# Kernel tuning notes

Hardware: AMD Instinct MI355X
Metric: run time of the kernel (lower is better)

## Reference

```python
import jax, jax.numpy as jnp
import numpy as np

EPS = 1e-6
CONV_P = 3.0
GM_P = 2.0
NUM_NODES = 50000
NUM_EDGES = 600000
NUM_GRAPHS = 512
IN_DIM = 128
HID = 128
OUT_DIM = 64


def _scatter_mean(vals, index, num_segments):
    # scatter_mean with empty segments -> 0 (count clamped to 1)
    s = jax.ops.segment_sum(vals, index, num_segments=num_segments)
    cnt = jax.ops.segment_sum(jnp.ones((vals.shape[0],), vals.dtype), index,
                              num_segments=num_segments)
    return s / jnp.maximum(cnt, 1.0)[:, None]


def _signed_pow(v, p):
    return jnp.sign(v) * (jnp.abs(v) + EPS) ** p


def _spm_conv(x, W, b, src, dst, p):
    h = x @ W.T + b                      # [N, hid] linear
    msg = h[src]                          # gather x_j  [E, hid]
    t = _signed_pow(msg, p)
    pooled = _scatter_mean(t, dst, NUM_NODES)
    return _signed_pow(pooled, 1.0 / p)


def setup_inputs() -> dict:
    key = jax.random.key(0)
    ks = jax.random.split(key, 8)
    x = jax.random.normal(ks[0], (NUM_NODES, IN_DIM), jnp.float32)
    edge_index = jax.random.randint(ks[1], (2, NUM_EDGES), 0, NUM_NODES)
    batch = jnp.sort(jax.random.randint(ks[2], (NUM_NODES,), 0, NUM_GRAPHS))
    s1 = 1.0 / np.sqrt(IN_DIM)
    s2 = 1.0 / np.sqrt(HID)
    W1 = jax.random.uniform(ks[3], (HID, IN_DIM), jnp.float32, -s1, s1)
    b1 = jax.random.uniform(ks[4], (HID,), jnp.float32, -s1, s1)
    W2 = jax.random.uniform(ks[5], (HID, HID), jnp.float32, -s2, s2)
    b2 = jax.random.uniform(ks[6], (HID,), jnp.float32, -s2, s2)
    # final layer: orthogonal-init frozen weight (out_dim=64, hid=128)
    A = jax.random.normal(ks[7], (HID, OUT_DIM), jnp.float32)
    Q, _ = jnp.linalg.qr(A)
    Wout = Q.T                            # [OUT_DIM, HID], orthonormal rows
    bout = jax.random.uniform(jax.random.fold_in(key, 9), (OUT_DIM,),
                              jnp.float32, -s2, s2)
    return {"x": x, "W1": W1, "b1": b1, "W2": W2, "b2": b2,
            "Wout": Wout, "bout": bout, "edge_index": edge_index,
            "batch": batch}


def reference(x, W1, b1, W2, b2, Wout, bout, edge_index, batch):
    src, dst = edge_index[0], edge_index[1]
    h = _spm_conv(x, W1, b1, src, dst, CONV_P)
    h = jax.nn.relu(h)                    # relu between conv layers only
    h = _spm_conv(h, W2, b2, src, dst, CONV_P)
    # global generalized mean pool (signed)
    t = _signed_pow(h, GM_P)
    pooled = _scatter_mean(t, batch, NUM_GRAPHS)
    graph_repr = _signed_pow(pooled, 1.0 / GM_P)   # [G, HID]
    return graph_repr @ Wout.T + bout              # [G, OUT_DIM]
```

## Files before the change

### kernel.cpp

```cpp
#include <hip/hip_runtime.h>
#include <hip/hip_bf16.h>
#include <math.h>

#define N_NODES 50000
#define N_EDGES 600000
#define N_GRAPHS 512
#define DIM 128
#define OUTD 64
#define EPSV 1e-6f
#define BSTRIDE 64

typedef __attribute__((ext_vector_type(8))) short bf16x8;
typedef __attribute__((ext_vector_type(4))) float f32x4;

__device__ __forceinline__ float sgn(float v) {
    return (v > 0.f) ? 1.f : ((v < 0.f) ? -1.f : 0.f);
}

__device__ __forceinline__ float cube_signed(float v) {
    float m = fabsf(v) + EPSV;
    return sgn(v) * m * m * m;
}

__device__ __forceinline__ float cbrt_pos(float m) {
    return exp2f(log2f(m) * (1.0f / 3.0f));
}

__device__ __forceinline__ unsigned short f2bf(float f) {
    unsigned u = __float_as_uint(f);
    unsigned r = (u + 0x7fff + ((u >> 16) & 1)) >> 16;
    return (unsigned short)r;
}

__device__ __forceinline__ float bf2f(unsigned short h) {
    return __uint_as_float(((unsigned)h) << 16);
}


__global__ void prep(const float* __restrict__ W1, const float* __restrict__ W2,
                     unsigned short* __restrict__ W1hi, unsigned short* __restrict__ W1lo,
                     unsigned short* __restrict__ W2hi, unsigned short* __restrict__ W2lo,
                     int* __restrict__ deg,
                     const int* __restrict__ batch, int* __restrict__ gstart) {
    int i = blockIdx.x * blockDim.x + threadIdx.x;
    if (i < N_NODES) deg[i] = 0;
    if (i < DIM * DIM) {
        float w = W1[i];
        unsigned short h = f2bf(w);
        W1hi[i] = h;
        W1lo[i] = f2bf(w - bf2f(h));
        w = W2[i];
        h = f2bf(w);
        W2hi[i] = h;
        W2lo[i] = f2bf(w - bf2f(h));
    }
    if (i <= N_GRAPHS) {
        int lo = 0, hi = N_NODES;
        while (lo < hi) {
            int mid = (lo + hi) >> 1;
            if (batch[mid] < i) lo = mid + 1; else hi = mid;
        }
        gstart[i] = lo;
    }
}


__global__ void bucket_fill(const int* __restrict__ src, const int* __restrict__ dst,
                            int* __restrict__ deg, int* __restrict__ csr, int E) {
    int e = blockIdx.x * blockDim.x + threadIdx.x;
    if (e < E) {
        int d = dst[e];
        int slot = atomicAdd(&deg[d], 1);
        if (slot < BSTRIDE) csr[d * BSTRIDE + slot] = src[e];
    }
}


__global__ __launch_bounds__(256) void linear_cube_mfma(const float* __restrict__ X,
                                                        const unsigned short* __restrict__ Whi,
                                                        const unsigned short* __restrict__ Wlo,
                                                        const float* __restrict__ B,
                                                        unsigned short* __restrict__ T) {
    int wave = threadIdx.x >> 6;
    int lane = threadIdx.x & 63;
    int tile = blockIdx.x * 4 + wave;
    if (tile >= N_NODES / 16) return;
    int n0 = tile * 16;
    int r = lane & 15;
    int g = lane >> 4;

    bf16x8 xh[4], xl[4];
    const float* xrow = X + (size_t)(n0 + r) * DIM + g * 8;
    #pragma unroll
    for (int kb = 0; kb < 4; kb++) {
        float4 a = *(const float4*)(xrow + kb * 32);
        float4 b = *(const float4*)(xrow + kb * 32 + 4);
        float v[8] = {a.x, a.y, a.z, a.w, b.x, b.y, b.z, b.w};
        #pragma unroll
        for (int j = 0; j < 8; j++) {
            unsigned short h = f2bf(v[j]);
            float rem = v[j] - bf2f(h);
            xh[kb][j] = (short)h;
            xl[kb][j] = (short)f2bf(rem);
        }
    }

    #pragma unroll
    for (int ct = 0; ct < 8; ct++) {
        const unsigned short* whbase = Whi + (size_t)(ct * 16 + r) * DIM + g * 8;
        const unsigned short* wlbase = Wlo + (size_t)(ct * 16 + r) * DIM + g * 8;
        f32x4 acc = {0.f, 0.f, 0.f, 0.f};
        #pragma unroll
        for (int kb = 0; kb < 4; kb++) {
            bf16x8 wh = *(const bf16x8*)(whbase + kb * 32);
            bf16x8 wl = *(const bf16x8*)(wlbase + kb * 32);
            acc = __builtin_amdgcn_mfma_f32_16x16x32_bf16(xh[kb], wh, acc, 0, 0, 0);
            acc = __builtin_amdgcn_mfma_f32_16x16x32_bf16(xl[kb], wh, acc, 0, 0, 0);
            acc = __builtin_amdgcn_mfma_f32_16x16x32_bf16(xh[kb], wl, acc, 0, 0, 0);
        }
        float bias = B[ct * 16 + r];
        #pragma unroll
        for (int q = 0; q < 4; q++) {
            int node = g * 4 + q;
            float h = acc[q] + bias;
            T[(size_t)(n0 + node) * DIM + ct * 16 + r] = f2bf(cube_signed(h));
        }
    }
}


__global__ __launch_bounds__(256) void aggregate(const unsigned* __restrict__ T32,
                                                 const int* __restrict__ deg,
                                                 const int* __restrict__ csr,
                                                 float* __restrict__ P, int relu) {
    int nd = blockIdx.x * 4 + (threadIdx.x >> 6);
    if (nd >= N_NODES) return;
    int lane = threadIdx.x & 63;
    int d = deg[nd];
    int cnt = d < BSTRIDE ? d : BSTRIDE;
    const int* bucket = csr + (size_t)nd * BSTRIDE;
    float a0 = 0.f, a1 = 0.f;
    int i = 0;
    for (; i + 4 <= cnt; i += 4) {
        int s0 = bucket[i], s1 = bucket[i + 1], s2 = bucket[i + 2], s3 = bucket[i + 3];
        unsigned u0 = T32[s0 * 64 + lane];
        unsigned u1 = T32[s1 * 64 + lane];
        unsigned u2 = T32[s2 * 64 + lane];
        unsigned u3 = T32[s3 * 64 + lane];
        a0 += __uint_as_float(u0 << 16) + __uint_as_float(u1 << 16)
            + __uint_as_float(u2 << 16) + __uint_as_float(u3 << 16);
        a1 += __uint_as_float(u0 & 0xffff0000u) + __uint_as_float(u1 & 0xffff0000u)
            + __uint_as_float(u2 & 0xffff0000u) + __uint_as_float(u3 & 0xffff0000u);
    }
    for (; i < cnt; i++) {
        unsigned u = T32[bucket[i] * 64 + lane];
        a0 += __uint_as_float(u << 16);
        a1 += __uint_as_float(u & 0xffff0000u);
    }
    float c = (float)(d > 1 ? d : 1);
    float m0 = a0 / c, m1 = a1 / c;
    float r0 = sgn(m0) * cbrt_pos(fabsf(m0) + EPSV);
    float r1 = sgn(m1) * cbrt_pos(fabsf(m1) + EPSV);
    if (relu) { r0 = fmaxf(r0, 0.f); r1 = fmaxf(r1, 0.f); }
    float2* dstp = (float2*)(P + (size_t)nd * DIM + lane * 2);
    *dstp = make_float2(r0, r1);
}


__global__ __launch_bounds__(128) void pool_final(const float* __restrict__ P,
                                                  const int* __restrict__ gstart,
                                                  const float* __restrict__ Wout,
                                                  const float* __restrict__ bout,
                                                  float* __restrict__ out) {
    __shared__ float R[DIM];
    __shared__ float partial[128];
    int g = blockIdx.x, f = threadIdx.x;
    int s = gstart[g], e = gstart[g + 1];
    float acc = 0.f;
    for (int i = s; i < e; i++) {
        float v = P[(size_t)i * DIM + f];
        float m = fabsf(v) + EPSV;
        acc += sgn(v) * m * m;
    }
    int cnt = e - s;
    float c = (float)(cnt > 1 ? cnt : 1);
    float mean = acc / c;
    R[f] = sgn(mean) * sqrtf(fabsf(mean) + EPSV);
    __syncthreads();

    int o = f & 63;
    int half = f >> 6;
    const float4* W4 = (const float4*)Wout + o * 32 + half * 16;
    const float4* R4 = (const float4*)R + half * 16;
    float a = 0.f;
    #pragma unroll
    for (int k = 0; k < 16; k++) {
        float4 w = W4[k];
        float4 r = R4[k];
        a += r.x * w.x + r.y * w.y + r.z * w.z + r.w * w.w;
    }
    partial[f] = a;
    __syncthreads();
    if (f < OUTD) out[(size_t)g * OUTD + f] = bout[f] + partial[f] + partial[f + 64];
}


extern "C" void kernel_launch(void* const* d_in, const int* in_sizes, int n_in,
                              void* d_out, int out_size, void* d_ws, size_t ws_size,
                              hipStream_t stream) {
    const float* x    = (const float*)d_in[0];
    const float* W1   = (const float*)d_in[1];
    const float* b1   = (const float*)d_in[2];
    const float* W2   = (const float*)d_in[3];
    const float* b2   = (const float*)d_in[4];
    const float* Wout = (const float*)d_in[5];
    const float* bout = (const float*)d_in[6];
    const int* edge   = (const int*)d_in[7];
    const int* batch  = (const int*)d_in[8];
    const int* srcp = edge;
    const int* dstp = edge + N_EDGES;
    float* out = (float*)d_out;

    char* ws = (char*)d_ws;
    size_t off = 0;
    auto alloc = [&](size_t bytes) -> char* {
        char* p = ws + off;
        off += (bytes + 255) / 256 * 256;
        return p;
    };
    unsigned short* T = (unsigned short*)alloc((size_t)N_NODES * DIM * 2);
    float* P        = (float*)alloc((size_t)N_NODES * DIM * 4);
    int*   deg      = (int*)alloc((size_t)N_NODES * 4);
    int*   csr      = (int*)alloc((size_t)N_NODES * BSTRIDE * 4);
    int*   gstart   = (int*)alloc((size_t)(N_GRAPHS + 1) * 4);
    unsigned short* W1hi = (unsigned short*)alloc((size_t)DIM * DIM * 2);
    unsigned short* W1lo = (unsigned short*)alloc((size_t)DIM * DIM * 2);
    unsigned short* W2hi = (unsigned short*)alloc((size_t)DIM * DIM * 2);
    unsigned short* W2lo = (unsigned short*)alloc((size_t)DIM * DIM * 2);

    prep<<<(N_NODES + 255) / 256, 256, 0, stream>>>(W1, W2, W1hi, W1lo, W2hi, W2lo,
                                                    deg, batch, gstart);
    bucket_fill<<<(N_EDGES + 255) / 256, 256, 0, stream>>>(srcp, dstp, deg, csr, N_EDGES);

    const int TILES = N_NODES / 16;
    const int LBLK = (TILES + 3) / 4;
    const int ABLK = (N_NODES + 3) / 4;
    linear_cube_mfma<<<LBLK, 256, 0, stream>>>(x, W1hi, W1lo, b1, T);
    aggregate<<<ABLK, 256, 0, stream>>>((const unsigned*)T, deg, csr, P, 1);
    linear_cube_mfma<<<LBLK, 256, 0, stream>>>(P, W2hi, W2lo, b2, T);
    aggregate<<<ABLK, 256, 0, stream>>>((const unsigned*)T, deg, csr, P, 0);
    pool_final<<<N_GRAPHS, 128, 0, stream>>>(P, gstart, Wout, bout, out);
}
```

Before: 219.4 us.

## Fuse first aggregation with second linear layer and merge setup kernels

Adds a kernel that gathers and mean-pools neighbour features for 16 nodes into shared memory, applies cube root and ReLU, then runs the second MFMA linear plus cube on that tile directly. This removes the fp32 round trip of the intermediate P between layers and one launch. Setup is also folded into one build kernel that handles bucket fill and weight splitting in separate block ranges, with deg zeroed by a memset. Each fused block now does both gather and MFMA work, which may change occupancy and latency hiding, and a second T buffer is used so the gather reads and the writes go to different arrays.

```diff
diff --git a/kernel.cpp b/kernel.cpp
--- a/kernel.cpp
+++ b/kernel.cpp
@@ -9,6 +9,8 @@
 #define OUTD 64
 #define EPSV 1e-6f
 #define BSTRIDE 64
+#define EBLK 2344
+#define PREP_BLK 64
 
 typedef __attribute__((ext_vector_type(8))) short bf16x8;
 typedef __attribute__((ext_vector_type(4))) float f32x4;
@@ -37,41 +39,40 @@
 }
 
 
-__global__ void prep(const float* __restrict__ W1, const float* __restrict__ W2,
-                     unsigned short* __restrict__ W1hi, unsigned short* __restrict__ W1lo,
-                     unsigned short* __restrict__ W2hi, unsigned short* __restrict__ W2lo,
-                     int* __restrict__ deg,
-                     const int* __restrict__ batch, int* __restrict__ gstart) {
-    int i = blockIdx.x * blockDim.x + threadIdx.x;
-    if (i < N_NODES) deg[i] = 0;
-    if (i < DIM * DIM) {
-        float w = W1[i];
-        unsigned short h = f2bf(w);
-        W1hi[i] = h;
-        W1lo[i] = f2bf(w - bf2f(h));
-        w = W2[i];
-        h = f2bf(w);
-        W2hi[i] = h;
-        W2lo[i] = f2bf(w - bf2f(h));
-    }
-    if (i <= N_GRAPHS) {
-        int lo = 0, hi = N_NODES;
-        while (lo < hi) {
-            int mid = (lo + hi) >> 1;
-            if (batch[mid] < i) lo = mid + 1; else hi = mid;
-        }
-        gstart[i] = lo;
-    }
-}
-
-
-__global__ void bucket_fill(const int* __restrict__ src, const int* __restrict__ dst,
-                            int* __restrict__ deg, int* __restrict__ csr, int E) {
-    int e = blockIdx.x * blockDim.x + threadIdx.x;
-    if (e < E) {
-        int d = dst[e];
-        int slot = atomicAdd(&deg[d], 1);
-        if (slot < BSTRIDE) csr[d * BSTRIDE + slot] = src[e];
+__global__ void build(const int* __restrict__ src, const int* __restrict__ dst,
+                      int* __restrict__ deg, int* __restrict__ csr,
+                      const float* __restrict__ W1, const float* __restrict__ W2,
+                      unsigned short* __restrict__ W1hi, unsigned short* __restrict__ W1lo,
+                      unsigned short* __restrict__ W2hi, unsigned short* __restrict__ W2lo,
+                      const int* __restrict__ batch, int* __restrict__ gstart) {
+    int b = blockIdx.x;
+    if (b < EBLK) {
+        int e = b * 256 + threadIdx.x;
+        if (e < N_EDGES) {
+            int d = dst[e];
+            int slot = atomicAdd(&deg[d], 1);
+            if (slot < BSTRIDE) csr[d * BSTRIDE + slot] = src[e];
+        }
+    } else {
+        int i = (b - EBLK) * 256 + threadIdx.x;
+        if (i < DIM * DIM) {
+            float w = W1[i];
+            unsigned short h = f2bf(w);
+            W1hi[i] = h;
+            W1lo[i] = f2bf(w - bf2f(h));
+            w = W2[i];
+            h = f2bf(w);
+            W2hi[i] = h;
+            W2lo[i] = f2bf(w - bf2f(h));
+        }
+        if (i <= N_GRAPHS) {
+            int lo = 0, hi = N_NODES;
+            while (lo < hi) {
+                int mid = (lo + hi) >> 1;
+                if (batch[mid] < i) lo = mid + 1; else hi = mid;
+            }
+            gstart[i] = lo;
+        }
     }
 }
 
@@ -129,10 +130,95 @@
 }
 
 
+__global__ __launch_bounds__(256) void agg_linear_cube(const unsigned* __restrict__ T32,
+                                                       const int* __restrict__ deg,
+                                                       const int* __restrict__ csr,
+                                                       const unsigned short* __restrict__ Whi,
+                                                       const unsigned short* __restrict__ Wlo,
+                                                       const float* __restrict__ B,
+                                                       unsigned short* __restrict__ Tout) {
+    __shared__ float Pl[16][132];
+    int wave = threadIdx.x >> 6;
+    int lane = threadIdx.x & 63;
+    int n0 = blockIdx.x * 16;
+
+    #pragma unroll
+    for (int q = 0; q < 4; q++) {
+        int nd = n0 + wave * 4 + q;
+        int d = deg[nd];
+        int cnt = d < BSTRIDE ? d : BSTRIDE;
+        const int* bucket = csr + (size_t)nd * BSTRIDE;
+        float a0 = 0.f, a1 = 0.f;
+        int i = 0;
+        for (; i + 4 <= cnt; i += 4) {
+            int s0 = bucket[i], s1 = bucket[i + 1], s2 = bucket[i + 2], s3 = bucket[i + 3];
+            unsigned u0 = T32[s0 * 64 + lane];
+            unsigned u1 = T32[s1 * 64 + lane];
+            unsigned u2 = T32[s2 * 64 + lane];
+            unsigned u3 = T32[s3 * 64 + lane];
+            a0 += __uint_as_float(u0 << 16) + __uint_as_float(u1 << 16)
+                + __uint_as_float(u2 << 16) + __uint_as_float(u3 << 16);
+            a1 += __uint_as_float(u0 & 0xffff0000u) + __uint_as_float(u1 & 0xffff0000u)
+                + __uint_as_float(u2 & 0xffff0000u) + __uint_as_float(u3 & 0xffff0000u);
+        }
+        for (; i < cnt; i++) {
+            unsigned u = T32[bucket[i] * 64 + lane];
+            a0 += __uint_as_float(u << 16);
+            a1 += __uint_as_float(u & 0xffff0000u);
+        }
+        float c = (float)(d > 1 ? d : 1);
+        float m0 = a0 / c, m1 = a1 / c;
+        float r0 = fmaxf(sgn(m0) * cbrt_pos(fabsf(m0) + EPSV), 0.f);
+        float r1 = fmaxf(sgn(m1) * cbrt_pos(fabsf(m1) + EPSV), 0.f);
+        int row = wave * 4 + q;
+        Pl[row][2 * lane]     = r0;
+        Pl[row][2 * lane + 1] = r1;
+    }
+    __syncthreads();
+
+    int r = lane & 15;
+    int g = lane >> 4;
+    bf16x8 xh[4], xl[4];
+    #pragma unroll
+    for (int kb = 0; kb < 4; kb++) {
+        const float* prow = &Pl[r][kb * 32 + g * 8];
+        #pragma unroll
+        for (int j = 0; j < 8; j++) {
+            float v = prow[j];
+            unsigned short h = f2bf(v);
+            xh[kb][j] = (short)h;
+            xl[kb][j] = (short)f2bf(v - bf2f(h));
+        }
+    }
+    #pragma unroll
+    for (int ctl = 0; ctl < 2; ctl++) {
+        int ct = wave * 2 + ctl;
+        const unsigned short* whbase = Whi + (size_t)(ct * 16 + r) * DIM + g * 8;
+        const unsigned short* wlbase = Wlo + (size_t)(ct * 16 + r) * DIM + g * 8;
+        f32x4 acc = {0.f, 0.f, 0.f, 0.f};
+        #pragma unroll
+        for (int kb = 0; kb < 4; kb++) {
+            bf16x8 wh = *(const bf16x8*)(whbase + kb * 32);
+            bf16x8 wl = *(const bf16x8*)(wlbase + kb * 32);
+            acc = __builtin_amdgcn_mfma_f32_16x16x32_bf16(xh[kb], wh, acc, 0, 0, 0);
+            acc = __builtin_amdgcn_mfma_f32_16x16x32_bf16(xl[kb], wh, acc, 0, 0, 0);
+            acc = __builtin_amdgcn_mfma_f32_16x16x32_bf16(xh[kb], wl, acc, 0, 0, 0);
+        }
+        float bias = B[ct * 16 + r];
+        #pragma unroll
+        for (int q = 0; q < 4; q++) {
+            int node = g * 4 + q;
+            float h = acc[q] + bias;
+            Tout[(size_t)(n0 + node) * DIM + ct * 16 + r] = f2bf(cube_signed(h));
+        }
+    }
+}
+
+
 __global__ __launch_bounds__(256) void aggregate(const unsigned* __restrict__ T32,
                                                  const int* __restrict__ deg,
                                                  const int* __restrict__ csr,
-                                                 float* __restrict__ P, int relu) {
+                                                 float* __restrict__ P) {
     int nd = blockIdx.x * 4 + (threadIdx.x >> 6);
     if (nd >= N_NODES) return;
     int lane = threadIdx.x & 63;
@@ -161,7 +247,6 @@
     float m0 = a0 / c, m1 = a1 / c;
     float r0 = sgn(m0) * cbrt_pos(fabsf(m0) + EPSV);
     float r1 = sgn(m1) * cbrt_pos(fabsf(m1) + EPSV);
-    if (relu) { r0 = fmaxf(r0, 0.f); r1 = fmaxf(r1, 0.f); }
     float2* dstp = (float2*)(P + (size_t)nd * DIM + lane * 2);
     *dstp = make_float2(r0, r1);
 }
@@ -228,7 +313,8 @@
         off += (bytes + 255) / 256 * 256;
         return p;
     };
-    unsigned short* T = (unsigned short*)alloc((size_t)N_NODES * DIM * 2);
+    unsigned short* T1 = (unsigned short*)alloc((size_t)N_NODES * DIM * 2);
+    unsigned short* T2 = (unsigned short*)alloc((size_t)N_NODES * DIM * 2);
     float* P        = (float*)alloc((size_t)N_NODES * DIM * 4);
     int*   deg      = (int*)alloc((size_t)N_NODES * 4);
     int*   csr      = (int*)alloc((size_t)N_NODES * BSTRIDE * 4);
@@ -238,16 +324,17 @@
     unsigned short* W2hi = (unsigned short*)alloc((size_t)DIM * DIM * 2);
     unsigned short* W2lo = (unsigned short*)alloc((size_t)DIM * DIM * 2);
 
-    prep<<<(N_NODES + 255) / 256, 256, 0, stream>>>(W1, W2, W1hi, W1lo, W2hi, W2lo,
-                                                    deg, batch, gstart);
-    bucket_fill<<<(N_EDGES + 255) / 256, 256, 0, stream>>>(srcp, dstp, deg, csr, N_EDGES);
+    hipMemsetAsync(deg, 0, (size_t)N_NODES * 4, stream);
+    build<<<EBLK + PREP_BLK, 256, 0, stream>>>(srcp, dstp, deg, csr,
+                                               W1, W2, W1hi, W1lo, W2hi, W2lo,
+                                               batch, gstart);
 
     const int TILES = N_NODES / 16;
     const int LBLK = (TILES + 3) / 4;
     const int ABLK = (N_NODES + 3) / 4;
-    linear_cube_mfma<<<LBLK, 256, 0, stream>>>(x, W1hi, W1lo, b1, T);
-    aggregate<<<ABLK, 256, 0, stream>>>((const unsigned*)T, deg, csr, P, 1);
-    linear_cube_mfma<<<LBLK, 256, 0, stream>>>(P, W2hi, W2lo, b2, T);
-    aggregate<<<ABLK, 256, 0, stream>>>((const unsigned*)T, deg, csr, P, 0);
+    linear_cube_mfma<<<LBLK, 256, 0, stream>>>(x, W1hi, W1lo, b1, T1);
+    agg_linear_cube<<<TILES, 256, 0, stream>>>((const unsigned*)T1, deg, csr,
+                                               W2hi, W2lo, b2, T2);
+    aggregate<<<ABLK, 256, 0, stream>>>((const unsigned*)T2, deg, csr, P);
     pool_final<<<N_GRAPHS, 128, 0, stream>>>(P, gstart, Wout, bout, out);
 }
```

Measured after the change: 210.4 us. -4.1%, faster.
